# Kernel optimization log

Measured on AMD Instinct MI355X. Metric: run time of the kernel, lower is better.

## Reference

```python
import math
import jax, jax.numpy as jnp
import numpy as np

# ---- module hyperparameters (from init_kwargs) ----
MAX_DISP = 48
IMG_WIDTH = 1248
W = IMG_WIDTH // 4          # 312 rows of the OT problem (left pixels)
C_COLS = MAX_DISP + W       # 360 columns (shifted right pixels)
NUM_ITER = 10
TAU = 0.95
EPS = 1.0
KAPPA = (1.0 - TAU) / 2.0
XI = (1.0 - TAU) / (1.0 + TAU)
RHO = EPS * TAU / (1.0 - TAU)
BIG_COST = 10000.0

B, H = 2, 64


def setup_inputs() -> dict:
    key = jax.random.key(0)
    scores = jax.random.normal(key, (B, MAX_DISP, H, W), dtype=jnp.float32)
    return {"scores": scores}


def _masked(x):
    # torch.where(isfinite(x), x, 0)
    return jnp.where(jnp.isfinite(x), x, jnp.zeros_like(x))


def _lse_kernel(Cm, f, g, axis):
    # S = (C - f[...,None] - g[...,None,:]) / eps ; eps*logsumexp(-S, axis)
    S = (Cm - f[..., None] - g[..., None, :]) / EPS
    w_res = EPS * jax.nn.logsumexp(-S, axis=axis)
    w_sgn = f if axis == -1 else g
    return w_res - _masked(w_sgn)


def _sinkhorn_update(Cm, f, g, axis, log_marginal):
    app = _lse_kernel(Cm, f, g, axis)
    return EPS * log_marginal - _masked(app)


def _smin(h, log_marginal):
    return -RHO * jax.nn.logsumexp(-h / RHO + log_marginal, axis=-1)


def _unbalanced_ot(Cm):
    # Cm: (B,H,W,C_COLS) cost matrix
    log_a = jnp.full((W,), -math.log(W), dtype=Cm.dtype)
    log_b = jnp.full((C_COLS,), -math.log(C_COLS), dtype=Cm.dtype)

    f = -EPS * jax.nn.logsumexp(-Cm / EPS + log_b, axis=-1)          # (B,H,W)
    g = jnp.zeros(Cm.shape[:2] + (C_COLS,), dtype=Cm.dtype)          # (B,H,C)

    for _ in range(NUM_ITER):
        old_f = f
        new_g = TAU * _sinkhorn_update(Cm, old_f, g, axis=-2, log_marginal=log_b)
        new_g = new_g - KAPPA * _smin(old_f, log_a)[..., None]
        new_g = new_g + XI * _smin(new_g, log_b)[..., None]
        new_f = TAU * _sinkhorn_update(Cm, f, new_g, axis=-1, log_marginal=log_a)
        new_f = new_f - KAPPA * _smin(new_g, log_b)[..., None]
        new_f = new_f + XI * _smin(new_f, log_a)[..., None]
        f, g = new_f, new_g

    S = (Cm - f[..., None] - g[..., None, :]) / EPS
    return jnp.exp(-S)                                               # transport plan P


def _scatter_to_cost(scores):
    # (B,D,H,W) scores -> (B,H,W,C_COLS) cost, vectorized scatter over d
    Bn, D, Hn, Wn = scores.shape
    j = jnp.arange(Wn)
    d = jnp.arange(D)
    col = j[None, :] - d[:, None] + MAX_DISP                          # (D,W), all in-range, no collisions
    jj = jnp.broadcast_to(j[None, :], (D, Wn))
    cost = jnp.full((Bn, Hn, Wn, C_COLS), BIG_COST, dtype=scores.dtype)
    # scores (B,D,H,W) -> (B,H,D,W) to match fancy-index result shape
    cost = cost.at[:, :, jj, col].set(-jnp.transpose(scores, (0, 2, 1, 3)))
    return cost


def _plan_to_disparity(P, D):
    right = jnp.arange(C_COLS, dtype=P.dtype) - D
    left = jnp.arange(W, dtype=P.dtype)
    disp_map = left[:, None] - right[None, :]                         # (W,C)
    mass = jnp.clip(jnp.sum(P, axis=-1), 1e-8, None)                  # (B,H,W)
    disp = jnp.sum(P * disp_map, axis=-1) / mass                      # (B,H,W)
    return disp[:, None, :, :]                                        # (B,1,H,W)


def reference(scores):
    D = scores.shape[1]
    Cm = _scatter_to_cost(scores)
    P = _unbalanced_ot(Cm)
    return _plan_to_disparity(P, D)
```

## Files before the change

kernel.cpp:

```cpp
#include <hip/hip_runtime.h>
#include <math.h>


typedef _Float16 half1;
typedef _Float16 half2v __attribute__((ext_vector_type(2)));

#define MAXD   48
#define WROWS  312
#define CCOLS  360
#define NITER  10
#define NT     384
#define NWAVE  6
#define NACC   21

__device__ __forceinline__ half2v h2(unsigned v) { return __builtin_bit_cast(half2v, v); }
__device__ __forceinline__ unsigned packf(float x, float y) {
    half2v v; v[0] = (half1)x; v[1] = (half1)y;
    return __builtin_bit_cast(unsigned, v);
}
__device__ __forceinline__ float fdot2(unsigned a, unsigned b, float c) {
    return __builtin_amdgcn_fdot2(h2(a), h2(b), c, false);
}
__device__ __forceinline__ float fdot2h(half2v a, unsigned b, float c) {
    return __builtin_amdgcn_fdot2(a, h2(b), c, false);
}
template <int CTRL>
__device__ __forceinline__ float dpp_add(float x, float acc) {
    int y = __builtin_amdgcn_update_dpp(0, __float_as_int(x), CTRL, 0xf, 0xf, true);
    return acc + __int_as_float(y);
}
__device__ __forceinline__ float dpp_sum64(float x) {
    x = dpp_add<0x111>(x, x);
    x = dpp_add<0x112>(x, x);
    x = dpp_add<0x114>(x, x);
    x = dpp_add<0x118>(x, x);
    x = dpp_add<0x142>(x, x);
    x = dpp_add<0x143>(x, x);
    return x;
}

__global__ __launch_bounds__(NT, 2)
void ot_disp_kernel(const float* __restrict__ scores, float* __restrict__ out) {
    const int tid = threadIdx.x;
    const int wid = tid >> 6;
    const int bid = blockIdx.x;
    const int b   = bid >> 6, h = bid & 63;

    const float LOG_A2 = -8.2854022f;
    const float LOG_B2 = -8.4918531f;
    const float TAU = 0.95f, KAPPA = 0.025f, XI = 0.025641026f;
    const float RHO = 19.0f, INVRHO = 0.052631579f, TIR = 0.05f;

    __shared__ unsigned EA2[204], EB2[204], GA2[180], GB2[181];
    __shared__ float s_red[NACC * NWAVE];
    half1* const EAh = (half1*)EA2;  half1* const EBh = (half1*)EB2;
    half1* const GAh = (half1*)GA2;  half1* const GBh = (half1*)GB2;

    if (tid < 24) { EA2[tid] = 0u; EA2[180 + tid] = 0u; EB2[tid] = 0u; }
    if (tid < 23) EB2[181 + tid] = 0u;
    if (tid == 30) { EBh[48] = (half1)0.f; EBh[361] = (half1)0.f; }

    const bool rowAct = (tid < WROWS);
    const bool colW   = (tid >= 1 && tid < CCOLS);
    const int  c = (tid < CCOLS) ? tid : (CCOLS - 1);
    const int  j = rowAct ? tid : (WROWS - 1);

    const float* src = scores + ((size_t)(b * MAXD) * 64 + h) * WROWS;
    const size_t dstr = (size_t)64 * WROWS;

    unsigned wcol[24];
    unsigned wrow[24];
    #pragma unroll
    for (int t = 0; t < 24; ++t) {
        int j0 = c - MAXD + 2 * t;
        int j1 = j0 + 1;
        bool v0 = (unsigned)j0 < (unsigned)WROWS;
        bool v1 = (unsigned)j1 < (unsigned)WROWS;
        float x0 = v0 ? __expf(src[(size_t)(2 * t) * dstr + (v0 ? j0 : 0)]) : 0.f;
        float x1 = v1 ? __expf(src[(size_t)(2 * t + 1) * dstr + (v1 ? j1 : 0)]) : 0.f;
        wcol[t] = packf(x0, x1);
    }
    #pragma unroll
    for (int t = 0; t < 24; ++t) {
        float x0 = __expf(src[(size_t)(47 - 2 * t) * dstr + j]);
        float x1 = __expf(src[(size_t)(46 - 2 * t) * dstr + j]);
        wrow[t] = packf(x0, x1);
    }

    const unsigned* const ecp = (c & 1) ? (EB2 + ((c + 1) >> 1)) : (EA2 + (c >> 1));
    const unsigned* const grp = (j & 1) ? (GA2 + ((j + 1) >> 1)) : (GB2 + ((j + 2) >> 1));

    const unsigned ONE2 = 0x3C003C00u;
    float y[NACC];
    {
        float s0 = 0.f, s1 = 0.f;
        #pragma unroll
        for (int t = 0; t < 24; t += 2) {
            s0 = fdot2(wrow[t], ONE2, s0);
            s1 = fdot2(wrow[t + 1], ONE2, s1);
        }
        float l  = __builtin_amdgcn_logf(s0 + s1);
        float e0 = __builtin_amdgcn_exp2f(-l);
        if (rowAct) { EAh[j + 48] = (half1)e0; EBh[j + 49] = (half1)e0; }
        y[0] = rowAct ? __builtin_amdgcn_exp2f(fmaf(INVRHO, l, LOG_A2)) : 0.f;
    }
    __syncthreads();

    float den = 0.f, ehv = 0.f;
    #pragma unroll
    for (int it = 0; it < NITER; ++it) {
        float a0 = 0.f, a1 = 0.f;
        #pragma unroll
        for (int t = 0; t < 24; t += 2) {
            a0 = fdot2(wcol[t],     ecp[t],     a0);
            a1 = fdot2(wcol[t + 1], ecp[t + 1], a1);
        }
        float lc = __builtin_amdgcn_logf(a0 + a1);
        float gh = __builtin_amdgcn_exp2f(-TAU * lc);
        if (colW) { GAh[c] = (half1)gh; GBh[c + 1] = (half1)gh; }
        y[1 + 2 * it] = colW ? __builtin_amdgcn_exp2f(fmaf(TIR, lc, LOG_B2)) : 0.f;
        __syncthreads();

        float b0 = 0.f, b1 = 0.f;
        #pragma unroll
        for (int t = 0; t < 24; t += 2) {
            b0 = fdot2(wrow[t],     grp[t],     b0);
            b1 = fdot2(wrow[t + 1], grp[t + 1], b1);
        }
        den = b0 + b1;
        float lr = __builtin_amdgcn_logf(den);
        ehv = __builtin_amdgcn_exp2f(-TAU * lr);
        if (rowAct) { EAh[j + 48] = (half1)ehv; EBh[j + 49] = (half1)ehv; }
        y[2 + 2 * it] = rowAct ? __builtin_amdgcn_exp2f(fmaf(TIR, lr, LOG_A2)) : 0.f;
        __syncthreads();
    }

    #pragma unroll
    for (int p = 0; p < NACC; ++p) {
        float s = dpp_sum64(y[p]);
        if ((tid & 63) == 63) s_red[p * NWAVE + wid] = s;
    }
    __syncthreads();

    float fsh = -LOG_B2, gsh = 0.f;
    {
        float R[NACC];
        #pragma unroll
        for (int p = 0; p < NACC; ++p) {
            const float* rp = s_red + p * NWAVE;
            float s = ((rp[0] + rp[1]) + (rp[2] + rp[3])) + (rp[4] + rp[5]);
            R[p] = __builtin_amdgcn_logf(s);
        }
        float sminF = fsh - RHO * R[0];
        #pragma unroll
        for (int it = 0; it < NITER; ++it) {
            float Cg = TAU * (LOG_B2 - fsh) - KAPPA * sminF;
            float sg = Cg - RHO * R[1 + 2 * it];
            gsh = Cg + XI * sg;
            float sminG = (1.f + XI) * sg;
            float Cf = TAU * (LOG_A2 - gsh) - KAPPA * sminG;
            float sf = Cf - RHO * R[2 + 2 * it];
            fsh = Cf + XI * sf;
            sminF = (1.f + XI) * sf;
        }
    }

    if (rowAct) {
        float n0 = 0.f, n1 = 0.f;
        #pragma unroll
        for (int t = 0; t < 24; ++t) {
            half2v dc; dc[0] = (half1)(float)(47 - 2 * t); dc[1] = (half1)(float)(46 - 2 * t);
            half2v wd = h2(wrow[t]) * dc;
            float& nn = (t & 1) ? n1 : n0;
            nn = fdot2h(wd, grp[t], nn);
        }
        float E = __builtin_amdgcn_exp2f(fsh + gsh) * ehv;
        float mass = fmaxf(E * den, 1e-8f);
        out[(size_t)bid * WROWS + j] = (E * (n0 + n1)) / mass;
    }
}

extern "C" void kernel_launch(void* const* d_in, const int* in_sizes, int n_in,
                              void* d_out, int out_size, void* d_ws, size_t ws_size,
                              hipStream_t stream) {
    const float* scores = (const float*)d_in[0];
    float* out = (float*)d_out;
    ot_disp_kernel<<<128, NT, 0, stream>>>(scores, out);
}
```

Before: 24.03 us.

## Give each wave a private row slab to drop one barrier per Sinkhorn iteration

Rows are repartitioned so each wave owns 52 rows and recomputes the column sums that feed those rows, with overlapping halos. Column g values then go into wave-private LDS, so only a lgkmcnt wait is needed between the column and row passes and one block barrier per iteration is removed. Column weights move from registers to LDS, and the E buffer is double-buffered so the next iteration's row writes cannot race with reads. The cost is redundant column work, LDS reads of the weights, and per-iteration DPP reductions in place of one batched reduction at the end.

After: 29.36 us. +22.2%, slower.

```diff
diff --git a/kernel.cpp b/kernel.cpp
--- a/kernel.cpp
+++ b/kernel.cpp
@@ -12,6 +12,8 @@
 #define NT     384
 #define NWAVE  6
 #define NACC   21
+#define WCS    25
+#define GSS    52
 
 __device__ __forceinline__ half2v h2(unsigned v) { return __builtin_bit_cast(half2v, v); }
 __device__ __forceinline__ unsigned packf(float x, float y) {
@@ -43,6 +45,7 @@
 void ot_disp_kernel(const float* __restrict__ scores, float* __restrict__ out) {
     const int tid = threadIdx.x;
     const int wid = tid >> 6;
+    const int L   = tid & 63;
     const int bid = blockIdx.x;
     const int b   = bid >> 6, h = bid & 63;
 
@@ -51,47 +54,50 @@
     const float TAU = 0.95f, KAPPA = 0.025f, XI = 0.025641026f;
     const float RHO = 19.0f, INVRHO = 0.052631579f, TIR = 0.05f;
 
-    __shared__ unsigned EA2[204], EB2[204], GA2[180], GB2[181];
+    __shared__ unsigned wC2[CCOLS * WCS];
+    __shared__ unsigned Ebuf[2][2][204];
+    __shared__ unsigned GSA[NWAVE * GSS], GSB[NWAVE * GSS];
     __shared__ float s_red[NACC * NWAVE];
-    half1* const EAh = (half1*)EA2;  half1* const EBh = (half1*)EB2;
-    half1* const GAh = (half1*)GA2;  half1* const GBh = (half1*)GB2;
-
-    if (tid < 24) { EA2[tid] = 0u; EA2[180 + tid] = 0u; EB2[tid] = 0u; }
-    if (tid < 23) EB2[181 + tid] = 0u;
-    if (tid == 30) { EBh[48] = (half1)0.f; EBh[361] = (half1)0.f; }
-
-    const bool rowAct = (tid < WROWS);
-    const bool colW   = (tid >= 1 && tid < CCOLS);
-    const int  c = (tid < CCOLS) ? tid : (CCOLS - 1);
-    const int  j = rowAct ? tid : (WROWS - 1);
 
     const float* src = scores + ((size_t)(b * MAXD) * 64 + h) * WROWS;
     const size_t dstr = (size_t)64 * WROWS;
 
-    unsigned wcol[24];
+    {
+        unsigned* ez = &Ebuf[0][0][0];
+        #pragma unroll
+        for (int k = 0; k < 3; ++k) {
+            int i = tid + k * NT;
+            if (i < 816) ez[i] = 0u;
+        }
+    }
+
+    #pragma unroll 1
+    for (int t = 0; t < 24; ++t) {
+        int c = tid;
+        if (c < CCOLS) {
+            int j0 = c - MAXD + 2 * t, j1 = j0 + 1;
+            bool v0 = (unsigned)j0 < (unsigned)WROWS;
+            bool v1 = (unsigned)j1 < (unsigned)WROWS;
+            float x0 = v0 ? __expf(src[(size_t)(2 * t) * dstr + (v0 ? j0 : 0)]) : 0.f;
+            float x1 = v1 ? __expf(src[(size_t)(2 * t + 1) * dstr + (v1 ? j1 : 0)]) : 0.f;
+            wC2[c * WCS + t] = packf(x0, x1);
+        }
+    }
+
+    const bool rowAct = (L < 52);
+    const int  j  = 52 * wid + (rowAct ? L : 51);
     unsigned wrow[24];
-    #pragma unroll
-    for (int t = 0; t < 24; ++t) {
-        int j0 = c - MAXD + 2 * t;
-        int j1 = j0 + 1;
-        bool v0 = (unsigned)j0 < (unsigned)WROWS;
-        bool v1 = (unsigned)j1 < (unsigned)WROWS;
-        float x0 = v0 ? __expf(src[(size_t)(2 * t) * dstr + (v0 ? j0 : 0)]) : 0.f;
-        float x1 = v1 ? __expf(src[(size_t)(2 * t + 1) * dstr + (v1 ? j1 : 0)]) : 0.f;
-        wcol[t] = packf(x0, x1);
-    }
-    #pragma unroll
-    for (int t = 0; t < 24; ++t) {
-        float x0 = __expf(src[(size_t)(47 - 2 * t) * dstr + j]);
-        float x1 = __expf(src[(size_t)(46 - 2 * t) * dstr + j]);
-        wrow[t] = packf(x0, x1);
-    }
-
-    const unsigned* const ecp = (c & 1) ? (EB2 + ((c + 1) >> 1)) : (EA2 + (c >> 1));
-    const unsigned* const grp = (j & 1) ? (GA2 + ((j + 1) >> 1)) : (GB2 + ((j + 2) >> 1));
+    {
+        const float rm = rowAct ? 1.f : 0.f;
+        #pragma unroll
+        for (int t = 0; t < 24; ++t) {
+            float x0 = rm * __expf(src[(size_t)(47 - 2 * t) * dstr + j]);
+            float x1 = rm * __expf(src[(size_t)(46 - 2 * t) * dstr + j]);
+            wrow[t] = packf(x0, x1);
+        }
+    }
 
     const unsigned ONE2 = 0x3C003C00u;
-    float y[NACC];
     {
         float s0 = 0.f, s1 = 0.f;
         #pragma unroll
@@ -101,46 +107,81 @@
         }
         float l  = __builtin_amdgcn_logf(s0 + s1);
         float e0 = __builtin_amdgcn_exp2f(-l);
-        if (rowAct) { EAh[j + 48] = (half1)e0; EBh[j + 49] = (half1)e0; }
-        y[0] = rowAct ? __builtin_amdgcn_exp2f(fmaf(INVRHO, l, LOG_A2)) : 0.f;
+        if (rowAct) {
+            ((half1*)Ebuf[0][0])[j + 48] = (half1)e0;
+            ((half1*)Ebuf[0][1])[j + 49] = (half1)e0;
+        }
+        float y0 = __builtin_amdgcn_exp2f(fmaf(INVRHO, l, LOG_A2));
+        float ts = dpp_sum64(y0);
+        if (L == 63) s_red[0 * NWAVE + wid] = ts;
     }
     __syncthreads();
 
+    const int  c0   = 52 * wid + 1 + L;
+    const bool v1   = (L < 35);
+    const int  cOff = v1 ? 64 : 0;
+    const int  par  = c0 & 1;
+    const int  bdw  = (c0 + par) >> 1;
+    const unsigned* const wc = wC2 + c0 * WCS;
+    const int  lo = (wid < 5) ? (60 * wid + 1) : 301;
+    const int  nn = (wid < 5) ? 60 : 59;
+    const bool own0 = (unsigned)(c0 - lo) < (unsigned)nn;
+    const bool own1 = v1 && ((unsigned)(c0 + 64 - lo) < (unsigned)nn);
+
+    half1* const gsA = (half1*)(GSA + wid * GSS);
+    half1* const gsB = (half1*)(GSB + wid * GSS);
+    const int Lr = rowAct ? L : 51;
+    const unsigned* const gp = (Lr & 1) ? (GSB + wid * GSS + ((Lr + 1) >> 1))
+                                        : (GSA + wid * GSS + (Lr >> 1));
+
     float den = 0.f, ehv = 0.f;
-    #pragma unroll
+    #pragma unroll 1
     for (int it = 0; it < NITER; ++it) {
-        float a0 = 0.f, a1 = 0.f;
+        const unsigned* ep = &Ebuf[it & 1][par][bdw];
+        float a0 = 0.f, a1 = 0.f, b0 = 0.f, b1 = 0.f;
+        const int eOff = cOff >> 1;
+        const int wOff = cOff * WCS ? (64 * WCS) : 0;
         #pragma unroll
         for (int t = 0; t < 24; t += 2) {
-            a0 = fdot2(wcol[t],     ecp[t],     a0);
-            a1 = fdot2(wcol[t + 1], ecp[t + 1], a1);
-        }
-        float lc = __builtin_amdgcn_logf(a0 + a1);
-        float gh = __builtin_amdgcn_exp2f(-TAU * lc);
-        if (colW) { GAh[c] = (half1)gh; GBh[c + 1] = (half1)gh; }
-        y[1 + 2 * it] = colW ? __builtin_amdgcn_exp2f(fmaf(TIR, lc, LOG_B2)) : 0.f;
-        __syncthreads();
-
-        float b0 = 0.f, b1 = 0.f;
+            a0 = fdot2(wc[t],     ep[t],     a0);
+            a1 = fdot2(wc[t + 1], ep[t + 1], a1);
+            b0 = fdot2(wc[t + (v1 ? 64 * WCS : 0)],     ep[t + eOff],     b0);
+            b1 = fdot2(wc[t + 1 + (v1 ? 64 * WCS : 0)], ep[t + 1 + eOff], b1);
+        }
+        float l0 = __builtin_amdgcn_logf(a0 + a1);
+        float l1 = __builtin_amdgcn_logf(b0 + b1);
+        float g0 = __builtin_amdgcn_exp2f(-TAU * l0);
+        float g1 = __builtin_amdgcn_exp2f(-TAU * l1);
+        gsA[L] = (half1)g0;
+        gsB[L + 1] = (half1)g0;
+        if (v1) { gsA[L + 64] = (half1)g1; gsB[L + 65] = (half1)g1; }
+        float yg = (own0 ? __builtin_amdgcn_exp2f(fmaf(TIR, l0, LOG_B2)) : 0.f)
+                 + (own1 ? __builtin_amdgcn_exp2f(fmaf(TIR, l1, LOG_B2)) : 0.f);
+        asm volatile("s_waitcnt lgkmcnt(0)" ::: "memory");
+        __builtin_amdgcn_sched_barrier(0);
+
+        float r0 = 0.f, r1 = 0.f;
         #pragma unroll
         for (int t = 0; t < 24; t += 2) {
-            b0 = fdot2(wrow[t],     grp[t],     b0);
-            b1 = fdot2(wrow[t + 1], grp[t + 1], b1);
-        }
-        den = b0 + b1;
+            r0 = fdot2(wrow[t],     gp[t],     r0);
+            r1 = fdot2(wrow[t + 1], gp[t + 1], r1);
+        }
+        den = r0 + r1;
         float lr = __builtin_amdgcn_logf(den);
         ehv = __builtin_amdgcn_exp2f(-TAU * lr);
-        if (rowAct) { EAh[j + 48] = (half1)ehv; EBh[j + 49] = (half1)ehv; }
-        y[2 + 2 * it] = rowAct ? __builtin_amdgcn_exp2f(fmaf(TIR, lr, LOG_A2)) : 0.f;
+        if (rowAct) {
+            ((half1*)Ebuf[(it + 1) & 1][0])[j + 48] = (half1)ehv;
+            ((half1*)Ebuf[(it + 1) & 1][1])[j + 49] = (half1)ehv;
+        }
+        float yf = __builtin_amdgcn_exp2f(fmaf(TIR, lr, LOG_A2));
+        float tg = dpp_sum64(yg);
+        float tf = dpp_sum64(yf);
+        if (L == 63) {
+            s_red[(1 + 2 * it) * NWAVE + wid] = tg;
+            s_red[(2 + 2 * it) * NWAVE + wid] = tf;
+        }
         __syncthreads();
     }
-
-    #pragma unroll
-    for (int p = 0; p < NACC; ++p) {
-        float s = dpp_sum64(y[p]);
-        if ((tid & 63) == 63) s_red[p * NWAVE + wid] = s;
-    }
-    __syncthreads();
 
     float fsh = -LOG_B2, gsh = 0.f;
     {
@@ -171,8 +212,8 @@
         for (int t = 0; t < 24; ++t) {
             half2v dc; dc[0] = (half1)(float)(47 - 2 * t); dc[1] = (half1)(float)(46 - 2 * t);
             half2v wd = h2(wrow[t]) * dc;
-            float& nn = (t & 1) ? n1 : n0;
-            nn = fdot2h(wd, grp[t], nn);
+            float& nnv = (t & 1) ? n1 : n0;
+            nnv = fdot2h(wd, gp[t], nnv);
         }
         float E = __builtin_amdgcn_exp2f(fsh + gsh) * ehv;
         float mass = fmaxf(E * den, 1e-8f);
```

## Compute needed column scalings per wave to drop one barrier per iteration

Applied to the files above, without the earlier changes.

Each wave now owns 52 rows and redundantly computes the 99 column potentials its rows depend on (two column slots per lane) into a private shared buffer. This removes the block-wide barrier between the column and row half-steps, leaving one barrier per iteration, with the row potentials double-buffered in shared memory. The cost is extra redundant column dot products, more registers (launch bounds lowered to one block per CU) and more accumulators per loop.

New measurement: 33.20 us. 38.2% more time.

```diff
diff --git a/kernel.cpp b/kernel.cpp
--- a/kernel.cpp
+++ b/kernel.cpp
@@ -12,6 +12,7 @@
 #define NT     384
 #define NWAVE  6
 #define NACC   21
+#define GSS    52
 
 __device__ __forceinline__ half2v h2(unsigned v) { return __builtin_bit_cast(half2v, v); }
 __device__ __forceinline__ unsigned packf(float x, float y) {
@@ -39,10 +40,11 @@
     return x;
 }
 
-__global__ __launch_bounds__(NT, 2)
+__global__ __launch_bounds__(NT, 1)
 void ot_disp_kernel(const float* __restrict__ scores, float* __restrict__ out) {
     const int tid = threadIdx.x;
     const int wid = tid >> 6;
+    const int L   = tid & 63;
     const int bid = blockIdx.x;
     const int b   = bid >> 6, h = bid & 63;
 
@@ -51,94 +53,141 @@
     const float TAU = 0.95f, KAPPA = 0.025f, XI = 0.025641026f;
     const float RHO = 19.0f, INVRHO = 0.052631579f, TIR = 0.05f;
 
-    __shared__ unsigned EA2[204], EB2[204], GA2[180], GB2[181];
+    __shared__ unsigned Ebuf[2][2][204];
+    __shared__ unsigned GS_A[NWAVE * GSS], GS_B[NWAVE * GSS];
     __shared__ float s_red[NACC * NWAVE];
-    half1* const EAh = (half1*)EA2;  half1* const EBh = (half1*)EB2;
-    half1* const GAh = (half1*)GA2;  half1* const GBh = (half1*)GB2;
-
-    if (tid < 24) { EA2[tid] = 0u; EA2[180 + tid] = 0u; EB2[tid] = 0u; }
-    if (tid < 23) EB2[181 + tid] = 0u;
-    if (tid == 30) { EBh[48] = (half1)0.f; EBh[361] = (half1)0.f; }
-
-    const bool rowAct = (tid < WROWS);
-    const bool colW   = (tid >= 1 && tid < CCOLS);
-    const int  c = (tid < CCOLS) ? tid : (CCOLS - 1);
-    const int  j = rowAct ? tid : (WROWS - 1);
+
+    if (tid < 48) {
+        int dw = (tid < 24) ? tid : (180 + tid - 24);
+        Ebuf[0][0][dw] = 0u; Ebuf[1][0][dw] = 0u;
+    } else if (tid < 95) {
+        int q = tid - 48;
+        int dw = (q < 24) ? q : (181 + q - 24);
+        Ebuf[0][1][dw] = 0u; Ebuf[1][1][dw] = 0u;
+    } else if (tid == 95) {
+        ((half1*)Ebuf[0][1])[48]  = (half1)0.f; ((half1*)Ebuf[1][1])[48]  = (half1)0.f;
+        ((half1*)Ebuf[0][1])[361] = (half1)0.f; ((half1*)Ebuf[1][1])[361] = (half1)0.f;
+    }
 
     const float* src = scores + ((size_t)(b * MAXD) * 64 + h) * WROWS;
     const size_t dstr = (size_t)64 * WROWS;
 
-    unsigned wcol[24];
-    unsigned wrow[24];
+    const bool rowAct = (L < 52);
+    const int  j   = 52 * wid + (rowAct ? L : 51);
+    const int  c0  = 52 * wid + 1 + L;
+    const bool v1  = (L < 35);
+
+    unsigned wc0[24], wc1[24], wrow[24];
     #pragma unroll
     for (int t = 0; t < 24; ++t) {
-        int j0 = c - MAXD + 2 * t;
-        int j1 = j0 + 1;
-        bool v0 = (unsigned)j0 < (unsigned)WROWS;
-        bool v1 = (unsigned)j1 < (unsigned)WROWS;
-        float x0 = v0 ? __expf(src[(size_t)(2 * t) * dstr + (v0 ? j0 : 0)]) : 0.f;
-        float x1 = v1 ? __expf(src[(size_t)(2 * t + 1) * dstr + (v1 ? j1 : 0)]) : 0.f;
-        wcol[t] = packf(x0, x1);
-    }
-    #pragma unroll
-    for (int t = 0; t < 24; ++t) {
-        float x0 = __expf(src[(size_t)(47 - 2 * t) * dstr + j]);
-        float x1 = __expf(src[(size_t)(46 - 2 * t) * dstr + j]);
-        wrow[t] = packf(x0, x1);
-    }
-
-    const unsigned* const ecp = (c & 1) ? (EB2 + ((c + 1) >> 1)) : (EA2 + (c >> 1));
-    const unsigned* const grp = (j & 1) ? (GA2 + ((j + 1) >> 1)) : (GB2 + ((j + 2) >> 1));
+        int ja = c0 - MAXD + 2 * t;
+        bool va = (unsigned)ja < (unsigned)WROWS;
+        bool vb = (unsigned)(ja + 1) < (unsigned)WROWS;
+        float x0 = va ? __expf(src[(size_t)(2 * t) * dstr + (va ? ja : 0)]) : 0.f;
+        float x1 = vb ? __expf(src[(size_t)(2 * t + 1) * dstr + (vb ? ja + 1 : 0)]) : 0.f;
+        wc0[t] = packf(x0, x1);
+        int jc = ja + 64;
+        bool vc = v1 && ((unsigned)jc < (unsigned)WROWS);
+        bool vd = v1 && ((unsigned)(jc + 1) < (unsigned)WROWS);
+        float x2 = vc ? __expf(src[(size_t)(2 * t) * dstr + (vc ? jc : 0)]) : 0.f;
+        float x3 = vd ? __expf(src[(size_t)(2 * t + 1) * dstr + (vd ? jc + 1 : 0)]) : 0.f;
+        wc1[t] = packf(x2, x3);
+    }
+    {
+        const float rm = rowAct ? 1.f : 0.f;
+        #pragma unroll
+        for (int t = 0; t < 24; ++t) {
+            float x0 = rm * __expf(src[(size_t)(47 - 2 * t) * dstr + j]);
+            float x1 = rm * __expf(src[(size_t)(46 - 2 * t) * dstr + j]);
+            wrow[t] = packf(x0, x1);
+        }
+    }
 
     const unsigned ONE2 = 0x3C003C00u;
     float y[NACC];
     {
-        float s0 = 0.f, s1 = 0.f;
-        #pragma unroll
-        for (int t = 0; t < 24; t += 2) {
-            s0 = fdot2(wrow[t], ONE2, s0);
-            s1 = fdot2(wrow[t + 1], ONE2, s1);
-        }
-        float l  = __builtin_amdgcn_logf(s0 + s1);
+        float s0=0,s1=0,s2=0,s3=0;
+        #pragma unroll
+        for (int t = 0; t < 24; t += 4) {
+            s0 = fdot2(wrow[t],   ONE2, s0);
+            s1 = fdot2(wrow[t+1], ONE2, s1);
+            s2 = fdot2(wrow[t+2], ONE2, s2);
+            s3 = fdot2(wrow[t+3], ONE2, s3);
+        }
+        float l  = __builtin_amdgcn_logf((s0+s1)+(s2+s3));
         float e0 = __builtin_amdgcn_exp2f(-l);
-        if (rowAct) { EAh[j + 48] = (half1)e0; EBh[j + 49] = (half1)e0; }
+        if (rowAct) {
+            ((half1*)Ebuf[0][0])[j + 48] = (half1)e0;
+            ((half1*)Ebuf[0][1])[j + 49] = (half1)e0;
+        }
         y[0] = rowAct ? __builtin_amdgcn_exp2f(fmaf(INVRHO, l, LOG_A2)) : 0.f;
     }
     __syncthreads();
+
+    const int par  = c0 & 1;
+    const int bdw  = (c0 + par) >> 1;
+    const int off1 = v1 ? 32 : 0;
+    half1* const gsA = (half1*)(GS_A + wid * GSS);
+    half1* const gsB = (half1*)(GS_B + wid * GSS);
+    const int Lr = rowAct ? L : 51;
+    const unsigned* const gp = (Lr & 1) ? (GS_B + wid * GSS + ((Lr + 1) >> 1))
+                                        : (GS_A + wid * GSS + (Lr >> 1));
+    const int lo = (wid < 5) ? (60 * wid + 1) : 301;
+    const int nn = (wid < 5) ? 60 : 59;
+    const bool own0 = (unsigned)(c0 - lo) < (unsigned)nn;
+    const bool own1 = v1 && ((unsigned)(c0 + 64 - lo) < (unsigned)nn);
 
     float den = 0.f, ehv = 0.f;
     #pragma unroll
     for (int it = 0; it < NITER; ++it) {
-        float a0 = 0.f, a1 = 0.f;
-        #pragma unroll
-        for (int t = 0; t < 24; t += 2) {
-            a0 = fdot2(wcol[t],     ecp[t],     a0);
-            a1 = fdot2(wcol[t + 1], ecp[t + 1], a1);
-        }
-        float lc = __builtin_amdgcn_logf(a0 + a1);
-        float gh = __builtin_amdgcn_exp2f(-TAU * lc);
-        if (colW) { GAh[c] = (half1)gh; GBh[c + 1] = (half1)gh; }
-        y[1 + 2 * it] = colW ? __builtin_amdgcn_exp2f(fmaf(TIR, lc, LOG_B2)) : 0.f;
-        __syncthreads();
-
-        float b0 = 0.f, b1 = 0.f;
-        #pragma unroll
-        for (int t = 0; t < 24; t += 2) {
-            b0 = fdot2(wrow[t],     grp[t],     b0);
-            b1 = fdot2(wrow[t + 1], grp[t + 1], b1);
-        }
-        den = b0 + b1;
+        const unsigned* ep = Ebuf[it & 1][par] + bdw;
+        float a0=0,a1=0,a2=0,a3=0, b0=0,b1=0,b2=0,b3=0;
+        #pragma unroll
+        for (int t = 0; t < 24; t += 4) {
+            a0 = fdot2(wc0[t],   ep[t],   a0);
+            a1 = fdot2(wc0[t+1], ep[t+1], a1);
+            a2 = fdot2(wc0[t+2], ep[t+2], a2);
+            a3 = fdot2(wc0[t+3], ep[t+3], a3);
+            b0 = fdot2(wc1[t],   ep[t+off1],   b0);
+            b1 = fdot2(wc1[t+1], ep[t+1+off1], b1);
+            b2 = fdot2(wc1[t+2], ep[t+2+off1], b2);
+            b3 = fdot2(wc1[t+3], ep[t+3+off1], b3);
+        }
+        float l0 = __builtin_amdgcn_logf((a0+a1)+(a2+a3));
+        float l1 = __builtin_amdgcn_logf((b0+b1)+(b2+b3));
+        float g0 = __builtin_amdgcn_exp2f(-TAU * l0);
+        float g1 = __builtin_amdgcn_exp2f(-TAU * l1);
+        gsA[L] = (half1)g0;
+        gsB[L + 1] = (half1)g0;
+        if (v1) { gsA[L + 64] = (half1)g1; gsB[L + 65] = (half1)g1; }
+        y[1 + 2*it] = (own0 ? __builtin_amdgcn_exp2f(fmaf(TIR, l0, LOG_B2)) : 0.f)
+                    + (own1 ? __builtin_amdgcn_exp2f(fmaf(TIR, l1, LOG_B2)) : 0.f);
+        asm volatile("s_waitcnt lgkmcnt(0)" ::: "memory");
+        __builtin_amdgcn_sched_barrier(0);
+
+        float r0=0,r1=0,r2=0,r3=0;
+        #pragma unroll
+        for (int t = 0; t < 24; t += 4) {
+            r0 = fdot2(wrow[t],   gp[t],   r0);
+            r1 = fdot2(wrow[t+1], gp[t+1], r1);
+            r2 = fdot2(wrow[t+2], gp[t+2], r2);
+            r3 = fdot2(wrow[t+3], gp[t+3], r3);
+        }
+        den = (r0+r1)+(r2+r3);
         float lr = __builtin_amdgcn_logf(den);
         ehv = __builtin_amdgcn_exp2f(-TAU * lr);
-        if (rowAct) { EAh[j + 48] = (half1)ehv; EBh[j + 49] = (half1)ehv; }
-        y[2 + 2 * it] = rowAct ? __builtin_amdgcn_exp2f(fmaf(TIR, lr, LOG_A2)) : 0.f;
+        if (rowAct) {
+            ((half1*)Ebuf[(it+1) & 1][0])[j + 48] = (half1)ehv;
+            ((half1*)Ebuf[(it+1) & 1][1])[j + 49] = (half1)ehv;
+        }
+        y[2 + 2*it] = rowAct ? __builtin_amdgcn_exp2f(fmaf(TIR, lr, LOG_A2)) : 0.f;
         __syncthreads();
     }
 
     #pragma unroll
     for (int p = 0; p < NACC; ++p) {
         float s = dpp_sum64(y[p]);
-        if ((tid & 63) == 63) s_red[p * NWAVE + wid] = s;
+        if (L == 63) s_red[p * NWAVE + wid] = s;
     }
     __syncthreads();
 
@@ -171,8 +220,8 @@
         for (int t = 0; t < 24; ++t) {
             half2v dc; dc[0] = (half1)(float)(47 - 2 * t); dc[1] = (half1)(float)(46 - 2 * t);
             half2v wd = h2(wrow[t]) * dc;
-            float& nn = (t & 1) ? n1 : n0;
-            nn = fdot2h(wd, grp[t], nn);
+            float& acc = (t & 1) ? n1 : n0;
+            acc = fdot2h(wd, gp[t], acc);
         }
         float E = __builtin_amdgcn_exp2f(fsh + gsh) * ehv;
         float mass = fmaxf(E * den, 1e-8f);
```
